# Optimization experiments

Measured on AMD Instinct MI355X. Metric: run time of the kernel, lower is better.

Reference implementation:

```python
import math
import jax, jax.numpy as jnp
import numpy as np
from jax import lax

# ---- static config (matches init_kwargs) ----
VOXEL = (0.075, 0.075)
PC = (-54.0, -54.0, -5.0, 54.0, 54.0, 3.0)
OSF = 8
POST_MAX = 500
FINAL_K = 300
MPK = 3
TASKS = [(1, 0), (2, 1), (2, 3), (1, 5), (2, 6), (2, 8)]  # (num_classes, label_offset)
H = W = 180
C_IN, C0, C1, C_NECK, C_HD = 256, 128, 256, 512, 64


def conv2d(x, w, b, stride=1, pad=1):
    y = lax.conv_general_dilated(x, w, (stride, stride), [(pad, pad), (pad, pad)],
                                 dimension_numbers=('NCHW', 'OIHW', 'NCHW'))
    return y + b[None, :, None, None]


def _gather_feat(feats, inds):  # feats [B,N,D], inds [B,K] -> [B,K,D]
    return jnp.take_along_axis(feats, inds[:, :, None], axis=1)


def _topk(scores, K):
    B, cat, Hh, Ww = scores.shape
    s, inds = lax.top_k(scores.reshape(B, cat, Hh * Ww), K)      # per-class topk [B,cat,K]
    ys = (inds // Ww).astype(jnp.float32)
    xs = (inds % Ww).astype(jnp.float32)
    s2, ind2 = lax.top_k(s.reshape(B, cat * K), K)               # cross-class topk [B,K]
    clses = ind2 // K
    g = lambda a: jnp.take_along_axis(a.reshape(B, cat * K), ind2, axis=1)
    return s2, g(inds), clses, g(ys), g(xs)


def _tg(feat, inds):  # transpose_and_gather: [B,C,H,W],[B,K] -> [B,K,C]
    B, C = feat.shape[0], feat.shape[1]
    return _gather_feat(feat.transpose(0, 2, 3, 1).reshape(B, -1, C), inds)


def decode_task(hm, reg, hei, dim_, rot, vel, label_offset):
    hm = jax.nn.sigmoid(hm)
    p = (MPK - 1) // 2
    hmax = lax.reduce_window(hm, -jnp.inf, lax.max, (1, 1, MPK, MPK), (1, 1, 1, 1),
                             [(0, 0), (0, 0), (p, p), (p, p)])
    hm = hm * (hmax == hm).astype(hm.dtype)                      # peak suppression
    scores, inds, clses, ys, xs = _topk(hm, POST_MAX)
    reg_g = _tg(reg, inds)
    hei_g = _tg(hei, inds)
    dim_g = jnp.exp(_tg(dim_, inds))                             # norm_bbox=True
    rot_g = _tg(rot, inds)
    vel_g = _tg(vel, inds)
    yaw = jnp.arctan2(rot_g[:, :, 0:1], rot_g[:, :, 1:2])
    xs = (xs[:, :, None] + reg_g[:, :, 0:1]) * OSF * VOXEL[0] + PC[0]
    ys = (ys[:, :, None] + reg_g[:, :, 1:2]) * OSF * VOXEL[1] + PC[1]
    boxes = jnp.concatenate([xs, ys, hei_g, dim_g, yaw, vel_g], axis=-1)  # [B,K,9]
    labels = clses.astype(jnp.float32) + label_offset
    return boxes, scores, labels


def grid_sample_bilinear(feat, xn, yn):  # feat [C,H,W]; xn,yn [K] normalized, align_corners=False
    C, Hh, Ww = feat.shape
    x = (xn + 1.0) * Ww / 2.0 - 0.5
    y = (yn + 1.0) * Hh / 2.0 - 0.5
    x0f = jnp.floor(x); y0f = jnp.floor(y)
    wx = x - x0f; wy = y - y0f
    x0 = x0f.astype(jnp.int32); y0 = y0f.astype(jnp.int32)
    ff = feat.reshape(C, Hh * Ww)
    def tap(xi, yi, wgt):
        valid = ((xi >= 0) & (xi < Ww) & (yi >= 0) & (yi < Hh)).astype(feat.dtype)
        idx = jnp.clip(yi, 0, Hh - 1) * Ww + jnp.clip(xi, 0, Ww - 1)
        return ff[:, idx] * (valid * wgt)[None, :]
    return (tap(x0, y0, (1 - wx) * (1 - wy)) + tap(x0 + 1, y0, wx * (1 - wy))
            + tap(x0, y0 + 1, (1 - wx) * wy) + tap(x0 + 1, y0 + 1, wx * wy))  # [C,K]


def pos2embed(pos, num_pos_feats=32):  # pos [K,7] -> [K, 7*num_pos_feats]
    pos = pos * (2.0 * math.pi)
    dim_t = jnp.arange(num_pos_feats, dtype=jnp.float32)
    dim_t = 2.0 * (dim_t // 2) / num_pos_feats + 1.0
    px = pos[..., None] / dim_t                                  # [K,7,F]
    e = jnp.stack([jnp.sin(px[..., 0::2]), jnp.cos(px[..., 1::2])], axis=-1)
    e = e.reshape(pos.shape[0], pos.shape[1], num_pos_feats)
    return e.reshape(pos.shape[0], -1)


def setup_inputs() -> dict:
    key = jax.random.key(0)
    def nrm(i, shape, scale=0.05):
        return jax.random.normal(jax.random.fold_in(key, i), shape, dtype=jnp.float32) * scale
    return {
        'bev_feat': jax.random.normal(jax.random.fold_in(key, 0), (1, C_IN, H, W), dtype=jnp.float32),
        'w_block0': nrm(1, (C0, C_IN, 3, 3)), 'b_block0': nrm(2, (C0,)),
        'w_block1': nrm(3, (C1, C0, 3, 3)), 'b_block1': nrm(4, (C1,)),
        'w_neck0': nrm(5, (256, C0, 1, 1)), 'b_neck0': nrm(6, (256,)),
        'w_neck1': nrm(7, (256, C1, 2, 2)), 'b_neck1': nrm(8, (256,)),
        'w_shared': nrm(9, (6, C_HD, C_NECK, 3, 3)), 'b_shared': nrm(10, (6, C_HD)),
        'w_hm': nrm(11, (6, 2, C_HD)), 'b_hm': nrm(12, (6, 2)),
        'w_reg': nrm(13, (6, 2, C_HD)), 'b_reg': nrm(14, (6, 2)),
        'w_hei': nrm(15, (6, 1, C_HD)), 'b_hei': nrm(16, (6, 1)),
        'w_dim': nrm(17, (6, 3, C_HD)), 'b_dim': nrm(18, (6, 3)),
        'w_rot': nrm(19, (6, 2, C_HD)), 'b_rot': nrm(20, (6, 2)),
        'w_vel': nrm(21, (6, 2, C_HD)), 'b_vel': nrm(22, (6, 2)),
        'w_pre': nrm(23, (C_NECK, C_NECK), 0.02), 'b_pre': nrm(24, (C_NECK,)),
        'w_qe': nrm(25, (C_NECK, C_NECK), 0.02), 'b_qe': nrm(26, (C_NECK,)),
        'w_qpe': nrm(27, (C_NECK, 224), 0.02), 'b_qpe': nrm(28, (C_NECK,)),
    }


def reference(bev_feat, w_block0, b_block0, w_block1, b_block1, w_neck0, b_neck0,
              w_neck1, b_neck1, w_shared, b_shared, w_hm, b_hm, w_reg, b_reg,
              w_hei, b_hei, w_dim, b_dim, w_rot, b_rot, w_vel, b_vel,
              w_pre, b_pre, w_qe, b_qe, w_qpe, b_qpe):
    # SECOND blocks
    x0 = jax.nn.relu(conv2d(bev_feat, w_block0, b_block0, 1, 1))        # [1,128,180,180]
    x1 = jax.nn.relu(conv2d(x0, w_block1, b_block1, 2, 1))              # [1,256,90,90]
    # neck: 1x1 lateral + 2x2/stride2 deconv, concat
    n0 = jax.nn.relu(conv2d(x0, w_neck0, b_neck0, 1, 0))                # [1,256,180,180]
    up = jnp.einsum('nihw,oiab->nohawb', x1, w_neck1).reshape(1, 256, H, W)
    n1 = jax.nn.relu(up + b_neck1[None, :, None, None])
    neck = jnp.concatenate([n0, n1], axis=1)                            # [1,512,180,180]
    # per-task heads + decode
    all_boxes, all_scores = [], []
    for t, (nc, off) in enumerate(TASKS):
        sh = jax.nn.relu(conv2d(neck, w_shared[t], b_shared[t], 1, 1))  # [1,64,180,180]
        head = lambda wt, bt: jnp.einsum('nchw,oc->nohw', sh, wt) + bt[None, :, None, None]
        hm = head(w_hm[t, :nc], b_hm[t, :nc])
        boxes, scores, _ = decode_task(hm, head(w_reg[t], b_reg[t]), head(w_hei[t], b_hei[t]),
                                       head(w_dim[t], b_dim[t]), head(w_rot[t], b_rot[t]),
                                       head(w_vel[t], b_vel[t]), off)
        all_boxes.append(boxes); all_scores.append(scores)
    boxes = jnp.concatenate(all_boxes, axis=1)                          # [1,3000,9]
    scores = jnp.concatenate(all_scores, axis=1)                        # [1,3000]
    top_s, idx = lax.top_k(scores, FINAL_K)
    boxes = jnp.take_along_axis(boxes, idx[:, :, None], axis=1)         # [1,300,9]
    scores = top_s
    query_xyz = boxes[:, :, :3]
    query_pred = jnp.concatenate([boxes[:, :, 3:9], scores[:, :, None]], axis=-1)  # [1,300,7]
    xn = (query_xyz[0, :, 0] - PC[0]) / (PC[3] - PC[0]) * 2.0 - 1.0
    yn = (query_xyz[0, :, 1] - PC[1]) / (PC[4] - PC[1]) * 2.0 - 1.0
    qf = grid_sample_bilinear(neck[0], xn, yn).T                        # [300,512]
    bev_flat = neck[0].reshape(C_NECK, -1).T                            # [32400,512]
    bev_out = bev_flat @ w_pre.T + b_pre + bev_flat
    qf_out = qf @ w_qe.T + b_qe + qf
    qf_out = qf_out + pos2embed(query_pred[0], 32) @ w_qpe.T + b_qpe
    return bev_out[None], qf_out[None], query_xyz[:1]
```

## Files before the change

### kernel.cpp

```cpp
#include <hip/hip_runtime.h>

typedef unsigned long long u64;
typedef unsigned int u32;

#define HW 32400
#define IMG 180
#define NTASK 6

__constant__ int c_nc[NTASK] = {1, 2, 2, 1, 2, 2};

#define GLL16(SRC, DST)                                                      \
    __builtin_amdgcn_global_load_lds(                                        \
        (const __attribute__((address_space(1))) unsigned int*)(SRC),        \
        (__attribute__((address_space(3))) unsigned int*)(DST), 16, 0, 0)

__global__ void zp_init_kernel(float* zp)
{
    zp[threadIdx.x] = 0.f;
}

__global__ __launch_bounds__(512) void conv3x3_relu_v12(
    const float* __restrict__ in, const float* __restrict__ wgt,
    const float* __restrict__ bias, float* __restrict__ out,
    const float* __restrict__ zp, int IC, int n_ocb)
{
    __shared__ float s_in[2][4080];
    __shared__ float s_w[2][432];

    int per = gridDim.x >> 3;
    int g = (blockIdx.x & 7) * per + (blockIdx.x >> 3);
    int sp = g / n_ocb;
    int ocb = g - sp * n_ocb;
    int oc0 = ocb * 16;
    int ty0 = (sp / 6) * 32, tx0 = (sp % 6) * 32;

    int tid = threadIdx.x;
    int sub = tid >> 8;
    int t8 = tid & 255;
    int xg = t8 & 7, y = t8 >> 3;
    int x = xg * 4;
    int sub8 = sub * 8;

    const int NC = (IC + 2) / 3;
    const int ic0_last = 3 * (NC - 1);

    int lane = tid & 63;
    int wv = tid >> 6;
    int dst0 = wv * 256;
    int dst1 = (wv + 8) * 256;
    const float* p0; int st0; bool last0;
    const float* p1; int st1; bool last1;
    bool ok1;
    {
        int e = dst0 + lane * 4;
        int icl = e / 1360; int r2 = e - icl * 1360;
        int rr = r2 / 40;   int cc = r2 - rr * 40;
        int gy = ty0 - 1 + rr, gx0 = tx0 - 4 + cc;
        bool geo = (unsigned)gy < 180u && (unsigned)gx0 < 180u;
        p0 = geo ? in + (size_t)icl * HW + (size_t)(gy * IMG + gx0) : zp;
        st0 = geo ? 3 * HW : 0;
        last0 = geo && (ic0_last + icl < IC);
    }
    {
        int e = dst1 + lane * 4;
        ok1 = e < 4080;
        int icl = e / 1360; int r2 = e - icl * 1360;
        int rr = r2 / 40;   int cc = r2 - rr * 40;
        int gy = ty0 - 1 + rr, gx0 = tx0 - 4 + cc;
        bool geo = ok1 && icl < 3 &&
                   (unsigned)gy < 180u && (unsigned)gx0 < 180u;
        p1 = geo ? in + (size_t)icl * HW + (size_t)(gy * IMG + gx0) : zp;
        st1 = geo ? 3 * HW : 0;
        last1 = geo && (ic0_last + icl < IC);
    }

    int wq = tid >> 4;
    int w_ic = wq / 9, w_tap = wq - w_ic * 9, w_oc = tid & 15;
    bool w_on = tid < 432;
    const float* wp = w_on
        ? wgt + ((size_t)(oc0 + w_oc) * IC + w_ic) * 9 + w_tap
        : wgt;
    bool w_last = w_on && (ic0_last + w_ic < IC);

    float acc[4][8];
#pragma unroll
    for (int p = 0; p < 4; ++p)
#pragma unroll
        for (int o = 0; o < 8; ++o) acc[p][o] = 0.f;

    {
        float wA = w_on ? *wp : 0.f;
        GLL16(p0, &s_in[0][0] + dst0);
        if (ok1) GLL16(p1, &s_in[0][0] + dst1);
        if (w_on) s_w[0][tid] = wA;
    }
    __syncthreads();

    const float* q0 = p0 + st0;
    const float* q1 = p1 + st1;
    const float* qw = wp + 27;

    for (int c = 0; c < NC; ++c) {
        int cur = c & 1;

        if (c + 1 < NC) {
            bool is_last = (c + 1 == NC - 1);
            float wN = 0.f;
            if (w_on) wN = (!is_last || w_last) ? *qw : 0.f;
            {
                const float* s0 = (!is_last || last0) ? q0 : zp;
                const float* s1 = (!is_last || last1) ? q1 : zp;
                GLL16(s0, &s_in[cur ^ 1][0] + dst0);
                if (ok1) GLL16(s1, &s_in[cur ^ 1][0] + dst1);
            }
            if (w_on) s_w[cur ^ 1][tid] = wN;
            q0 += st0; q1 += st1; qw += 27;
        }

        {
            const float* sbuf = &s_in[cur][0];
            const float* swb = &s_w[cur][0];
#pragma unroll
            for (int ic = 0; ic < 3; ++ic) {
#pragma unroll
                for (int dy = 0; dy < 3; ++dy) {
                    const float* rowp = sbuf + ic * 1360 + (y + dy) * 40 + x;
                    float2 a0 = *(const float2*)(rowp + 2);
                    float4 a1 = *(const float4*)(rowp + 4);
                    float2 a2 = *(const float2*)(rowp + 8);
                    float v[6] = {a0.y, a1.x, a1.y, a1.z, a1.w, a2.x};
#pragma unroll
                    for (int dx = 0; dx < 3; ++dx) {
                        const float* wpp =
                            swb + (ic * 9 + dy * 3 + dx) * 16 + sub8;
                        float4 w0 = *(const float4*)(wpp + 0);
                        float4 w1 = *(const float4*)(wpp + 4);
                        float wvv[8] = {w0.x, w0.y, w0.z, w0.w,
                                        w1.x, w1.y, w1.z, w1.w};
#pragma unroll
                        for (int p = 0; p < 4; ++p) {
                            float vv = v[p + dx];
                            float* ar = acc[p];
#pragma unroll
                            for (int o = 0; o < 8; ++o)
                                ar[o] = fmaf(vv, wvv[o], ar[o]);
                        }
                    }
                }
            }
        }
        __syncthreads();
    }

    int gy = ty0 + y, gx0 = tx0 + x;
    if (gy < IMG && gx0 < IMG) {
#pragma unroll
        for (int o = 0; o < 8; ++o) {
            float b = bias[oc0 + sub8 + o];
            float4 r;
            r.x = acc[0][o] + b;
            r.y = acc[1][o] + b;
            r.z = acc[2][o] + b;
            r.w = acc[3][o] + b;
            r.x = r.x > 0.f ? r.x : 0.f;
            r.y = r.y > 0.f ? r.y : 0.f;
            r.z = r.z > 0.f ? r.z : 0.f;
            r.w = r.w > 0.f ? r.w : 0.f;
            *(float4*)&out[(size_t)(oc0 + sub8 + o) * HW + gy * IMG + gx0] = r;
        }
    }
}

__global__ __launch_bounds__(256) void conv3x3s2_relu_v2(
    const float* __restrict__ in, const float* __restrict__ wgt,
    const float* __restrict__ bias, float* __restrict__ out)
{
    __shared__ float s_in[2][31][34];
    __shared__ float s_w[2][9][16];

    int sp = blockIdx.x; int ocb = blockIdx.y;
    int oty0 = (sp / 6) * 15, otx0 = (sp % 6) * 15;
    int iy0 = 2 * oty0 - 1, ix0 = 2 * otx0 - 1;
    int tid = threadIdx.x;
    int tx = tid & 15, ty = tid >> 4;
    bool active = (tx < 15) && (ty < 15);

    float acc[16];
#pragma unroll
    for (int o = 0; o < 16; ++o) acc[o] = 0.f;

    for (int ic0 = 0; ic0 < 128; ic0 += 2) {
        __syncthreads();
        for (int e = tid; e < 2 * 31 * 31; e += 256) {
            int ic = e / 961; int rem = e - ic * 961;
            int rr = rem / 31; int cc = rem - rr * 31;
            int gy = iy0 + rr, gx = ix0 + cc;
            float v = 0.f;
            if ((unsigned)gy < 180u && (unsigned)gx < 180u)
                v = in[(size_t)(ic0 + ic) * HW + gy * IMG + gx];
            s_in[ic][rr][cc] = v;
        }
        for (int e = tid; e < 288; e += 256) {
            int oc = e & 15; int tap = (e >> 4) % 9; int ic = e / 144;
            s_w[ic][tap][oc] =
                wgt[((size_t)(ocb * 16 + oc) * 128 + ic0 + ic) * 9 + tap];
        }
        __syncthreads();
        if (!active) continue;
#pragma unroll
        for (int ic = 0; ic < 2; ++ic) {
#pragma unroll
            for (int tap = 0; tap < 9; ++tap) {
                int dy = tap / 3, dx = tap - dy * 3;
                float v = s_in[ic][2 * ty + dy][2 * tx + dx];
                float4 w0 = *(const float4*)&s_w[ic][tap][0];
                float4 w1 = *(const float4*)&s_w[ic][tap][4];
                float4 w2 = *(const float4*)&s_w[ic][tap][8];
                float4 w3 = *(const float4*)&s_w[ic][tap][12];
                float wv[16] = {w0.x, w0.y, w0.z, w0.w, w1.x, w1.y, w1.z, w1.w,
                                w2.x, w2.y, w2.z, w2.w, w3.x, w3.y, w3.z, w3.w};
#pragma unroll
                for (int o = 0; o < 16; ++o) acc[o] = fmaf(v, wv[o], acc[o]);
            }
        }
    }
    if (active) {
        int yy = oty0 + ty, xx = otx0 + tx;
#pragma unroll
        for (int o = 0; o < 16; ++o) {
            float r = acc[o] + bias[ocb * 16 + o];
            out[(size_t)(ocb * 16 + o) * 8100 + yy * 90 + xx] =
                r > 0.f ? r : 0.f;
        }
    }
}

__global__ __launch_bounds__(256) void conv1x1_relu_kernel(
    const float* __restrict__ in, const float* __restrict__ w,
    const float* __restrict__ bias, float* __restrict__ out)
{
    __shared__ float s_x[8][256];
    __shared__ float s_w[8][16];
    int p0 = blockIdx.x * 256; int ocb = blockIdx.y;
    int tid = threadIdx.x;
    float acc[16];
#pragma unroll
    for (int o = 0; o < 16; ++o) acc[o] = 0.f;

    for (int ic0 = 0; ic0 < 128; ic0 += 8) {
        for (int e = tid; e < 2048; e += 256) {
            int ic = e >> 8; int p = e & 255;
            s_x[ic][p] = (p0 + p < HW) ? in[(size_t)(ic0 + ic) * HW + p0 + p] : 0.f;
        }
        for (int e = tid; e < 128; e += 256) {
            int ic = e >> 4; int oc = e & 15;
            s_w[ic][oc] = w[(size_t)(ocb * 16 + oc) * 128 + ic0 + ic];
        }
        __syncthreads();
#pragma unroll
        for (int ic = 0; ic < 8; ++ic) {
            float v = s_x[ic][tid];
            float4 w0 = *(const float4*)&s_w[ic][0];
            float4 w1 = *(const float4*)&s_w[ic][4];
            float4 w2 = *(const float4*)&s_w[ic][8];
            float4 w3 = *(const float4*)&s_w[ic][12];
            float wv[16] = {w0.x, w0.y, w0.z, w0.w, w1.x, w1.y, w1.z, w1.w,
                            w2.x, w2.y, w2.z, w2.w, w3.x, w3.y, w3.z, w3.w};
#pragma unroll
            for (int o = 0; o < 16; ++o) acc[o] = fmaf(v, wv[o], acc[o]);
        }
        __syncthreads();
    }
    int p = p0 + tid;
    if (p < HW) {
#pragma unroll
        for (int o = 0; o < 16; ++o) {
            float r = acc[o] + bias[ocb * 16 + o];
            out[(size_t)(ocb * 16 + o) * HW + p] = r > 0.f ? r : 0.f;
        }
    }
}

__global__ __launch_bounds__(256) void deconv2x2_relu_kernel(
    const float* __restrict__ in, const float* __restrict__ wgt,
    const float* __restrict__ bias, float* __restrict__ out)
{
    __shared__ float s_x[8][256];
    __shared__ float s_w[8][4][16];
    int p0 = blockIdx.x * 256; int ocb = blockIdx.y;
    int tid = threadIdx.x;
    float acc[4][16];
#pragma unroll
    for (int ab = 0; ab < 4; ++ab)
#pragma unroll
        for (int o = 0; o < 16; ++o) acc[ab][o] = 0.f;

    for (int ic0 = 0; ic0 < 256; ic0 += 8) {
        for (int e = tid; e < 2048; e += 256) {
            int ic = e >> 8; int p = e & 255;
            s_x[ic][p] = (p0 + p < 8100) ? in[(size_t)(ic0 + ic) * 8100 + p0 + p] : 0.f;
        }
        for (int e = tid; e < 512; e += 256) {
            int oc = e & 15; int ab = (e >> 4) & 3; int ic = e >> 6;
            s_w[ic][ab][oc] =
                wgt[((size_t)(ocb * 16 + oc) * 256 + ic0 + ic) * 4 + ab];
        }
        __syncthreads();
#pragma unroll
        for (int ic = 0; ic < 8; ++ic) {
            float v = s_x[ic][tid];
#pragma unroll
            for (int ab = 0; ab < 4; ++ab) {
                float4 w0 = *(const float4*)&s_w[ic][ab][0];
                float4 w1 = *(const float4*)&s_w[ic][ab][4];
                float4 w2 = *(const float4*)&s_w[ic][ab][8];
                float4 w3 = *(const float4*)&s_w[ic][ab][12];
                float wv[16] = {w0.x, w0.y, w0.z, w0.w, w1.x, w1.y, w1.z, w1.w,
                                w2.x, w2.y, w2.z, w2.w, w3.x, w3.y, w3.z, w3.w};
#pragma unroll
                for (int o = 0; o < 16; ++o)
                    acc[ab][o] = fmaf(v, wv[o], acc[ab][o]);
            }
        }
        __syncthreads();
    }
    int sp = p0 + tid;
    if (sp < 8100) {
        int sy = sp / 90, sx = sp - sy * 90;
#pragma unroll
        for (int ab = 0; ab < 4; ++ab) {
            int a = ab >> 1, bb = ab & 1;
            int Y = 2 * sy + a, X = 2 * sx + bb;
#pragma unroll
            for (int o = 0; o < 16; ++o) {
                float r = acc[ab][o] + bias[ocb * 16 + o];
                out[(size_t)(ocb * 16 + o) * HW + Y * IMG + X] = r > 0.f ? r : 0.f;
            }
        }
    }
}

__global__ __launch_bounds__(256) void heads_kernel(
    const float* __restrict__ sh,
    const float* __restrict__ w_hm, const float* __restrict__ b_hm,
    const float* __restrict__ w_reg, const float* __restrict__ b_reg,
    const float* __restrict__ w_hei, const float* __restrict__ b_hei,
    const float* __restrict__ w_dim, const float* __restrict__ b_dim,
    const float* __restrict__ w_rot, const float* __restrict__ b_rot,
    const float* __restrict__ w_vel, const float* __restrict__ b_vel,
    float* __restrict__ hm_sig, float* __restrict__ heads)
{
    __shared__ float s_w[64][12];
    __shared__ float s_b[12];
    int t = blockIdx.y;
    int tid = threadIdx.x;
    for (int e = tid; e < 768; e += 256) {
        int c = e / 12; int r = e - c * 12;
        float v;
        if (r < 2)       v = w_hm [(t * 2 + r) * 64 + c];
        else if (r < 4)  v = w_reg[(t * 2 + r - 2) * 64 + c];
        else if (r < 5)  v = w_hei[t * 64 + c];
        else if (r < 8)  v = w_dim[(t * 3 + r - 5) * 64 + c];
        else if (r < 10) v = w_rot[(t * 2 + r - 8) * 64 + c];
        else             v = w_vel[(t * 2 + r - 10) * 64 + c];
        s_w[c][r] = v;
    }
    if (tid < 12) {
        int r = tid; float v;
        if (r < 2)       v = b_hm [t * 2 + r];
        else if (r < 4)  v = b_reg[t * 2 + r - 2];
        else if (r < 5)  v = b_hei[t];
        else if (r < 8)  v = b_dim[t * 3 + r - 5];
        else if (r < 10) v = b_rot[t * 2 + r - 8];
        else             v = b_vel[t * 2 + r - 10];
        s_b[r] = v;
    }
    __syncthreads();
    int p = blockIdx.x * 256 + tid;
    if (p >= HW) return;
    float a[12];
#pragma unroll
    for (int r = 0; r < 12; ++r) a[r] = 0.f;
    const float* shp = sh + (size_t)t * 64 * HW + p;
    for (int c = 0; c < 64; ++c) {
        float x = shp[(size_t)c * HW];
        float4 w0 = *(const float4*)&s_w[c][0];
        float4 w1 = *(const float4*)&s_w[c][4];
        float4 w2 = *(const float4*)&s_w[c][8];
        float wv[12] = {w0.x, w0.y, w0.z, w0.w, w1.x, w1.y, w1.z, w1.w,
                        w2.x, w2.y, w2.z, w2.w};
#pragma unroll
        for (int r = 0; r < 12; ++r) a[r] = fmaf(x, wv[r], a[r]);
    }
#pragma unroll
    for (int r = 0; r < 12; ++r) a[r] += s_b[r];
    hm_sig[(size_t)(t * 2 + 0) * HW + p] = 1.f / (1.f + expf(-a[0]));
    hm_sig[(size_t)(t * 2 + 1) * HW + p] = 1.f / (1.f + expf(-a[1]));
#pragma unroll
    for (int r = 0; r < 10; ++r)
        heads[(size_t)(t * 10 + r) * HW + p] = a[2 + r];
}

__global__ __launch_bounds__(256) void nms_key_kernel(
    const float* __restrict__ hm_sig, u64* __restrict__ keys)
{
    int t = blockIdx.y;
    int i = blockIdx.x * 256 + threadIdx.x;
    int nc = c_nc[t];
    u64 key = 0;
    if (i < nc * HW) {
        int c = i / HW; int p = i - c * HW;
        int y = p / IMG; int x = p - y * IMG;
        const float* base = hm_sig + (size_t)(t * 2 + c) * HW;
        float s = base[p];
        float m = s;
#pragma unroll
        for (int dy = -1; dy <= 1; ++dy)
#pragma unroll
            for (int dx = -1; dx <= 1; ++dx) {
                int yy = y + dy, xx = x + dx;
                if ((unsigned)yy < 180u && (unsigned)xx < 180u)
                    m = fmaxf(m, base[yy * IMG + xx]);
            }
        float sm = (s == m) ? s : 0.f;
        key = ((u64)__float_as_uint(sm) << 32) | (u64)(u32)(~(u32)i);
    }
    keys[(size_t)t * 65536 + i] = key;
}

template <int N, int T>
__device__ void bitonic_sort_desc(u64* s)
{
    const int tid = threadIdx.x;
    for (int k = 2; k <= N; k <<= 1) {
        for (int j = k >> 1; j > 0; j >>= 1) {
            __syncthreads();
            for (int idx = tid; idx < N / 2; idx += T) {
                int i = ((idx & ~(j - 1)) << 1) | (idx & (j - 1));
                int l = i | j;
                u64 a = s[i], b = s[l];
                bool sw = ((i & k) == 0) ? (a < b) : (a > b);
                if (sw) { s[i] = b; s[l] = a; }
            }
        }
    }
    __syncthreads();
}

__global__ __launch_bounds__(256) void topk_stage1_kernel(
    const u64* __restrict__ keys, u64* __restrict__ cand)
{
    __shared__ u64 s[4096];
    int t = blockIdx.y, ch = blockIdx.x;
    const u64* src = keys + (size_t)t * 65536 + ch * 4096;
    for (int i = threadIdx.x; i < 4096; i += 256) s[i] = src[i];
    bitonic_sort_desc<4096, 256>(s);
    u64* dst = cand + ((size_t)t * 16 + ch) * 512;
    for (int i = threadIdx.x; i < 512; i += 256) dst[i] = s[i];
}

__global__ __launch_bounds__(512) void topk_stage2_kernel(
    const u64* __restrict__ cand, u64* __restrict__ top_keys)
{
    extern __shared__ u64 s2[];
    int t = blockIdx.x;
    for (int i = threadIdx.x; i < 8192; i += 512) s2[i] = cand[(size_t)t * 8192 + i];
    bitonic_sort_desc<8192, 512>(s2);
    for (int i = threadIdx.x; i < 500; i += 512) top_keys[t * 500 + i] = s2[i];
}

__global__ __launch_bounds__(256) void final_decode_kernel(
    const u64* __restrict__ top_keys, const float* __restrict__ heads,
    float* __restrict__ qxyz, float* __restrict__ qpred)
{
    __shared__ u64 s[4096];
    int tid = threadIdx.x;
    for (int i = tid; i < 4096; i += 256) {
        u64 v = 0;
        if (i < 3000) {
            u64 k = top_keys[i];
            v = (k & 0xFFFFFFFF00000000ull) | (u64)(u32)(~(u32)i);
        }
        s[i] = v;
    }
    bitonic_sort_desc<4096, 256>(s);
    for (int q = tid; q < 300; q += 256) {
        u64 k2 = s[q];
        u32 gpos = ~(u32)(k2 & 0xFFFFFFFFull);
        int t = gpos / 500;
        u64 ok = top_keys[gpos];
        float score = __uint_as_float((u32)(ok >> 32));
        u32 comb = ~(u32)(ok & 0xFFFFFFFFull);
        int p = (int)(comb % HW);
        int yy = p / IMG, xx = p - yy * IMG;
        const float* hd = heads + (size_t)t * 10 * HW;
        float reg0 = hd[0 * HW + p], reg1 = hd[1 * HW + p], hei = hd[2 * HW + p];
        float d0 = expf(hd[3 * HW + p]);
        float d1 = expf(hd[4 * HW + p]);
        float d2 = expf(hd[5 * HW + p]);
        float rot0 = hd[6 * HW + p], rot1 = hd[7 * HW + p];
        float vel0 = hd[8 * HW + p], vel1 = hd[9 * HW + p];
        float yaw = atan2f(rot0, rot1);
        float X = ((float)xx + reg0) * 8.0f * 0.075f + (-54.0f);
        float Y = ((float)yy + reg1) * 8.0f * 0.075f + (-54.0f);
        qxyz[q * 3 + 0] = X;
        qxyz[q * 3 + 1] = Y;
        qxyz[q * 3 + 2] = hei;
        qpred[q * 7 + 0] = d0; qpred[q * 7 + 1] = d1; qpred[q * 7 + 2] = d2;
        qpred[q * 7 + 3] = yaw; qpred[q * 7 + 4] = vel0; qpred[q * 7 + 5] = vel1;
        qpred[q * 7 + 6] = score;
    }
}

__global__ __launch_bounds__(256) void sample_embed_kernel(
    const float* __restrict__ neck, const float* __restrict__ qxyz,
    const float* __restrict__ qpred, float* __restrict__ qf,
    float* __restrict__ emb)
{
    int q = blockIdx.x;
    int tid = threadIdx.x;
    float X = qxyz[q * 3 + 0], Y = qxyz[q * 3 + 1];
    float xn = (X - (-54.0f)) / 108.0f * 2.0f - 1.0f;
    float yn = (Y - (-54.0f)) / 108.0f * 2.0f - 1.0f;
    float gx = (xn + 1.0f) * 180.0f / 2.0f - 0.5f;
    float gy = (yn + 1.0f) * 180.0f / 2.0f - 0.5f;
    float x0f = floorf(gx), y0f = floorf(gy);
    float wx = gx - x0f, wy = gy - y0f;
    int x0 = (int)x0f, y0 = (int)y0f;
    int xs[4] = {x0, x0 + 1, x0, x0 + 1};
    int ys[4] = {y0, y0, y0 + 1, y0 + 1};
    float wt[4] = {(1.f - wx) * (1.f - wy), wx * (1.f - wy),
                   (1.f - wx) * wy, wx * wy};
    int idx[4]; float wv[4];
#pragma unroll
    for (int k = 0; k < 4; ++k) {
        bool valid = xs[k] >= 0 && xs[k] < IMG && ys[k] >= 0 && ys[k] < IMG;
        int cx = xs[k] < 0 ? 0 : (xs[k] > IMG - 1 ? IMG - 1 : xs[k]);
        int cy = ys[k] < 0 ? 0 : (ys[k] > IMG - 1 ? IMG - 1 : ys[k]);
        idx[k] = cy * IMG + cx;
        wv[k] = valid ? wt[k] : 0.f;
    }
    for (int c = tid; c < 512; c += 256) {
        const float* f = neck + (size_t)c * HW;
        float v = f[idx[0]] * wv[0] + f[idx[1]] * wv[1] +
                  f[idx[2]] * wv[2] + f[idx[3]] * wv[3];
        qf[q * 512 + c] = v;
    }
    if (tid < 224) {
        int fidx = tid >> 5; int j = tid & 31; int m = j >> 1;
        float pos = qpred[q * 7 + fidx] * 6.283185307179586f;
        float dt = 2.0f * (float)m / 32.0f + 1.0f;
        float v = pos / dt;
        emb[q * 224 + tid] = (j & 1) ? cosf(v) : sinf(v);
    }
}

__global__ __launch_bounds__(256) void qfout_kernel(
    const float* __restrict__ qf, const float* __restrict__ emb,
    const float* __restrict__ w_qe, const float* __restrict__ b_qe,
    const float* __restrict__ w_qpe, const float* __restrict__ b_qpe,
    float* __restrict__ outq)
{
    int g = blockIdx.x * 256 + threadIdx.x;
    if (g >= 300 * 512) return;
    int q = g >> 9, o = g & 511;
    const float* qrow = qf + q * 512;
    const float* wrow = w_qe + (size_t)o * 512;
    float acc = 0.f;
    for (int c = 0; c < 512; ++c) acc = fmaf(qrow[c], wrow[c], acc);
    const float* erow = emb + q * 224;
    const float* wr2 = w_qpe + (size_t)o * 224;
    float acc2 = 0.f;
    for (int j = 0; j < 224; ++j) acc2 = fmaf(erow[j], wr2[j], acc2);
    outq[g] = acc + b_qe[o] + qrow[o] + acc2 + b_qpe[o];
}

__global__ __launch_bounds__(256) void bev_out_kernel(
    const float* __restrict__ neck, const float* __restrict__ w_pre,
    const float* __restrict__ b_pre, float* __restrict__ outb)
{
    __shared__ float sA[16][132];
    __shared__ float sB[16][132];
    int per = gridDim.x >> 3;
    int g = (blockIdx.x & 7) * per + (blockIdx.x >> 3);
    int pt = g >> 2; int ob = g & 3;
    int p0 = pt * 128, o0 = ob * 128;
    int tid = threadIdx.x, tx = tid & 15, ty = tid >> 4;
    float acc[8][8];
#pragma unroll
    for (int i = 0; i < 8; ++i)
#pragma unroll
        for (int j = 0; j < 8; ++j) acc[i][j] = 0.f;

    for (int c0 = 0; c0 < 512; c0 += 16) {
        for (int e = tid; e < 2048; e += 256) {
            int k = e >> 7, p = e & 127;
            int gp = p0 + p;
            sA[k][p] = gp < HW ? neck[(size_t)(c0 + k) * HW + gp] : 0.f;
        }
        for (int e4 = tid; e4 < 512; e4 += 256) {
            int o = e4 >> 2, kk = e4 & 3;
            float4 v = *(const float4*)&w_pre[(size_t)(o0 + o) * 512 + c0 + kk * 4];
            sB[kk * 4 + 0][o] = v.x; sB[kk * 4 + 1][o] = v.y;
            sB[kk * 4 + 2][o] = v.z; sB[kk * 4 + 3][o] = v.w;
        }
        __syncthreads();
#pragma unroll
        for (int k = 0; k < 16; ++k) {
            float4 a0 = *(const float4*)&sA[k][ty * 4];
            float4 a1 = *(const float4*)&sA[k][64 + ty * 4];
            float4 b0 = *(const float4*)&sB[k][tx * 4];
            float4 b1 = *(const float4*)&sB[k][64 + tx * 4];
            float av[8] = {a0.x, a0.y, a0.z, a0.w, a1.x, a1.y, a1.z, a1.w};
            float bv[8] = {b0.x, b0.y, b0.z, b0.w, b1.x, b1.y, b1.z, b1.w};
#pragma unroll
            for (int i = 0; i < 8; ++i)
#pragma unroll
                for (int j = 0; j < 8; ++j)
                    acc[i][j] = fmaf(av[i], bv[j], acc[i][j]);
        }
        __syncthreads();
    }
#pragma unroll
    for (int i = 0; i < 8; ++i) {
        int pl = (i < 4) ? (ty * 4 + i) : (64 + ty * 4 + i - 4);
        int p = p0 + pl;
        if (p >= HW) continue;
#pragma unroll
        for (int j = 0; j < 8; ++j) {
            int ol = (j < 4) ? (tx * 4 + j) : (64 + tx * 4 + j - 4);
            int o = o0 + ol;
            outb[(size_t)p * 512 + o] =
                acc[i][j] + b_pre[o] + neck[(size_t)o * HW + p];
        }
    }
}

extern "C" void kernel_launch(void* const* d_in, const int* in_sizes, int n_in,
                              void* d_out, int out_size, void* d_ws, size_t ws_size,
                              hipStream_t stream)
{
    (void)in_sizes; (void)n_in; (void)out_size; (void)ws_size;

    const float* bev   = (const float*)d_in[0];
    const float* w_b0  = (const float*)d_in[1];
    const float* b_b0  = (const float*)d_in[2];
    const float* w_b1  = (const float*)d_in[3];
    const float* b_b1  = (const float*)d_in[4];
    const float* w_n0  = (const float*)d_in[5];
    const float* b_n0  = (const float*)d_in[6];
    const float* w_n1  = (const float*)d_in[7];
    const float* b_n1  = (const float*)d_in[8];
    const float* w_sh  = (const float*)d_in[9];
    const float* b_sh  = (const float*)d_in[10];
    const float* w_hm  = (const float*)d_in[11];
    const float* b_hm  = (const float*)d_in[12];
    const float* w_reg = (const float*)d_in[13];
    const float* b_reg = (const float*)d_in[14];
    const float* w_hei = (const float*)d_in[15];
    const float* b_hei = (const float*)d_in[16];
    const float* w_dim = (const float*)d_in[17];
    const float* b_dim = (const float*)d_in[18];
    const float* w_rot = (const float*)d_in[19];
    const float* b_rot = (const float*)d_in[20];
    const float* w_vel = (const float*)d_in[21];
    const float* b_vel = (const float*)d_in[22];
    const float* w_pre = (const float*)d_in[23];
    const float* b_pre = (const float*)d_in[24];
    const float* w_qe  = (const float*)d_in[25];
    const float* b_qe  = (const float*)d_in[26];
    const float* w_qpe = (const float*)d_in[27];
    const float* b_qpe = (const float*)d_in[28];

    float* out = (float*)d_out;
    float* wsf = (float*)d_ws;

    float* x0    = wsf;
    float* x1    = x0 + (size_t)128 * HW;
    float* neck  = x1 + (size_t)256 * 8100;
    float* sh    = neck + (size_t)512 * HW;
    float* heads = sh + (size_t)NTASK * 64 * HW;
    float* hm    = heads + (size_t)NTASK * 10 * HW;
    float* qpred = hm + (size_t)NTASK * 2 * HW;
    float* qf    = qpred + 300 * 7;
    float* emb   = qf + 300 * 512;
    u64* keys    = (u64*)(emb + 300 * 224);
    u64* cand    = keys + (size_t)NTASK * 65536;
    u64* topk    = cand + (size_t)NTASK * 16 * 512;
    float* zp    = (float*)(((uintptr_t)(topk + 3008) + 63) & ~(uintptr_t)63);

    float* out_bev = out;
    float* out_qf  = out + (size_t)HW * 512;
    float* out_xyz = out + (size_t)HW * 512 + 300 * 512;

    zp_init_kernel<<<dim3(1), dim3(64), 0, stream>>>(zp);

    conv3x3_relu_v12<<<dim3(288), dim3(512), 0, stream>>>(
        bev, w_b0, b_b0, x0, zp, 256, 8);
    conv3x3s2_relu_v2<<<dim3(36, 16), dim3(256), 0, stream>>>(
        x0, w_b1, b_b1, x1);
    conv1x1_relu_kernel<<<dim3(127, 16), dim3(256), 0, stream>>>(
        x0, w_n0, b_n0, neck);
    deconv2x2_relu_kernel<<<dim3(32, 16), dim3(256), 0, stream>>>(
        x1, w_n1, b_n1, neck + (size_t)256 * HW);
    conv3x3_relu_v12<<<dim3(864), dim3(512), 0, stream>>>(
        neck, w_sh, b_sh, sh, zp, 512, 24);
    heads_kernel<<<dim3(127, 6), dim3(256), 0, stream>>>(
        sh, w_hm, b_hm, w_reg, b_reg, w_hei, b_hei, w_dim, b_dim,
        w_rot, b_rot, w_vel, b_vel, hm, heads);
    nms_key_kernel<<<dim3(256, 6), dim3(256), 0, stream>>>(hm, keys);
    topk_stage1_kernel<<<dim3(16, 6), dim3(256), 0, stream>>>(keys, cand);
    topk_stage2_kernel<<<dim3(6), dim3(512), 65536, stream>>>(cand, topk);
    final_decode_kernel<<<dim3(1), dim3(256), 0, stream>>>(
        topk, heads, out_xyz, qpred);
    sample_embed_kernel<<<dim3(300), dim3(256), 0, stream>>>(
        neck, out_xyz, qpred, qf, emb);
    qfout_kernel<<<dim3(600), dim3(256), 0, stream>>>(
        qf, emb, w_qe, b_qe, w_qpe, b_qpe, out_qf);
    bev_out_kernel<<<dim3(1016), dim3(256), 0, stream>>>(
        neck, w_pre, b_pre, out_bev);
}
```

Before: 3.998 ms.

## Repack conv3x3 weights and read them from global instead of LDS staging

Adds a repack kernel that reorders the 3x3 conv weights into a [ocb][ic][tap][16] layout for both 3x3 convs. The conv kernel then reads weights straight from global memory with wave-uniform addresses. This drops the per-chunk LDS weight staging and its store traffic. In exchange it adds a weight-repack pass on every call and relies on the cache and scalar path serving repeated weight reads efficiently.

Result: slower. 4.427 ms (+10.7%).

```diff
diff --git a/kernel.cpp b/kernel.cpp
--- a/kernel.cpp
+++ b/kernel.cpp
@@ -19,13 +19,25 @@
     zp[threadIdx.x] = 0.f;
 }
 
-__global__ __launch_bounds__(512) void conv3x3_relu_v12(
-    const float* __restrict__ in, const float* __restrict__ wgt,
+__global__ __launch_bounds__(256) void repack_w_kernel(
+    const float* __restrict__ w, float* __restrict__ rp, int IC, int total)
+{
+    int i = blockIdx.x * 256 + threadIdx.x;
+    if (i >= total) return;
+    int o = i & 15;
+    int tap = (i >> 4) % 9;
+    int rest = i / 144;
+    int ic = rest % IC;
+    int ocb = rest / IC;
+    rp[i] = w[((size_t)(ocb * 16 + o) * IC + ic) * 9 + tap];
+}
+
+__global__ __launch_bounds__(512) void conv3x3_relu_v13(
+    const float* __restrict__ in, const float* __restrict__ rp,
     const float* __restrict__ bias, float* __restrict__ out,
     const float* __restrict__ zp, int IC, int n_ocb)
 {
     __shared__ float s_in[2][4080];
-    __shared__ float s_w[2][432];
 
     int per = gridDim.x >> 3;
     int g = (blockIdx.x & 7) * per + (blockIdx.x >> 3);
@@ -42,12 +54,12 @@
     int sub8 = sub * 8;
 
     const int NC = (IC + 2) / 3;
-    const int ic0_last = 3 * (NC - 1);
 
     int lane = tid & 63;
     int wv = tid >> 6;
     int dst0 = wv * 256;
     int dst1 = (wv + 8) * 256;
+    const int ic0_last = 3 * (NC - 1);
     const float* p0; int st0; bool last0;
     const float* p1; int st1; bool last1;
     bool ok1;
@@ -74,13 +86,7 @@
         last1 = geo && (ic0_last + icl < IC);
     }
 
-    int wq = tid >> 4;
-    int w_ic = wq / 9, w_tap = wq - w_ic * 9, w_oc = tid & 15;
-    bool w_on = tid < 432;
-    const float* wp = w_on
-        ? wgt + ((size_t)(oc0 + w_oc) * IC + w_ic) * 9 + w_tap
-        : wgt;
-    bool w_last = w_on && (ic0_last + w_ic < IC);
+    const float* wb = rp + (size_t)ocb * IC * 144 + sub8;
 
     float acc[4][8];
 #pragma unroll
@@ -88,38 +94,28 @@
 #pragma unroll
         for (int o = 0; o < 8; ++o) acc[p][o] = 0.f;
 
-    {
-        float wA = w_on ? *wp : 0.f;
-        GLL16(p0, &s_in[0][0] + dst0);
-        if (ok1) GLL16(p1, &s_in[0][0] + dst1);
-        if (w_on) s_w[0][tid] = wA;
-    }
+    GLL16(p0, &s_in[0][0] + dst0);
+    if (ok1) GLL16(p1, &s_in[0][0] + dst1);
     __syncthreads();
 
     const float* q0 = p0 + st0;
     const float* q1 = p1 + st1;
-    const float* qw = wp + 27;
 
     for (int c = 0; c < NC; ++c) {
         int cur = c & 1;
 
         if (c + 1 < NC) {
             bool is_last = (c + 1 == NC - 1);
-            float wN = 0.f;
-            if (w_on) wN = (!is_last || w_last) ? *qw : 0.f;
-            {
-                const float* s0 = (!is_last || last0) ? q0 : zp;
-                const float* s1 = (!is_last || last1) ? q1 : zp;
-                GLL16(s0, &s_in[cur ^ 1][0] + dst0);
-                if (ok1) GLL16(s1, &s_in[cur ^ 1][0] + dst1);
-            }
-            if (w_on) s_w[cur ^ 1][tid] = wN;
-            q0 += st0; q1 += st1; qw += 27;
+            const float* s0 = (!is_last || last0) ? q0 : zp;
+            const float* s1 = (!is_last || last1) ? q1 : zp;
+            GLL16(s0, &s_in[cur ^ 1][0] + dst0);
+            if (ok1) GLL16(s1, &s_in[cur ^ 1][0] + dst1);
+            q0 += st0; q1 += st1;
         }
 
         {
             const float* sbuf = &s_in[cur][0];
-            const float* swb = &s_w[cur][0];
+            const float* wc = wb + (size_t)(c * 3) * 144;
 #pragma unroll
             for (int ic = 0; ic < 3; ++ic) {
 #pragma unroll
@@ -131,8 +127,7 @@
                     float v[6] = {a0.y, a1.x, a1.y, a1.z, a1.w, a2.x};
 #pragma unroll
                     for (int dx = 0; dx < 3; ++dx) {
-                        const float* wpp =
-                            swb + (ic * 9 + dy * 3 + dx) * 16 + sub8;
+                        const float* wpp = wc + (ic * 9 + dy * 3 + dx) * 16;
                         float4 w0 = *(const float4*)(wpp + 0);
                         float4 w1 = *(const float4*)(wpp + 4);
                         float wvv[8] = {w0.x, w0.y, w0.z, w0.w,
@@ -688,23 +683,33 @@
     u64* cand    = keys + (size_t)NTASK * 65536;
     u64* topk    = cand + (size_t)NTASK * 16 * 512;
     float* zp    = (float*)(((uintptr_t)(topk + 3008) + 63) & ~(uintptr_t)63);
+    float* rp0   = zp + 64;
+    float* rpsh  = rp0 + (size_t)8 * 256 * 144 + 8192;
 
     float* out_bev = out;
     float* out_qf  = out + (size_t)HW * 512;
     float* out_xyz = out + (size_t)HW * 512 + 300 * 512;
 
     zp_init_kernel<<<dim3(1), dim3(64), 0, stream>>>(zp);
-
-    conv3x3_relu_v12<<<dim3(288), dim3(512), 0, stream>>>(
-        bev, w_b0, b_b0, x0, zp, 256, 8);
+    {
+        int tot0 = 8 * 256 * 144;
+        repack_w_kernel<<<dim3((tot0 + 255) / 256), dim3(256), 0, stream>>>(
+            w_b0, rp0, 256, tot0);
+        int tot1 = 24 * 512 * 144;
+        repack_w_kernel<<<dim3((tot1 + 255) / 256), dim3(256), 0, stream>>>(
+            w_sh, rpsh, 512, tot1);
+    }
+
+    conv3x3_relu_v13<<<dim3(288), dim3(512), 0, stream>>>(
+        bev, rp0, b_b0, x0, zp, 256, 8);
     conv3x3s2_relu_v2<<<dim3(36, 16), dim3(256), 0, stream>>>(
         x0, w_b1, b_b1, x1);
     conv1x1_relu_kernel<<<dim3(127, 16), dim3(256), 0, stream>>>(
         x0, w_n0, b_n0, neck);
     deconv2x2_relu_kernel<<<dim3(32, 16), dim3(256), 0, stream>>>(
         x1, w_n1, b_n1, neck + (size_t)256 * HW);
-    conv3x3_relu_v12<<<dim3(864), dim3(512), 0, stream>>>(
-        neck, w_sh, b_sh, sh, zp, 512, 24);
+    conv3x3_relu_v13<<<dim3(864), dim3(512), 0, stream>>>(
+        neck, rpsh, b_sh, sh, zp, 512, 24);
     heads_kernel<<<dim3(127, 6), dim3(256), 0, stream>>>(
         sh, w_hm, b_hm, w_reg, b_reg, w_hei, b_hei, w_dim, b_dim,
         w_rot, b_rot, w_vel, b_vel, hm, heads);
```
